# Performance work log

Measured on AMD Instinct MI355X. Metric: run time of the kernel, lower is better.

The kernel has to match this reference:

```python
import jax, jax.numpy as jnp
import numpy as np

N_HEAD = 16
SPARSITY_K = 64


def _apply_rope(x):
    # x: [B, H, T, D]
    D = x.shape[-1]
    T = x.shape[-2]
    freqs = 1.0 / (10000.0 ** (jnp.arange(0, D, 2, dtype=jnp.float32) / D))  # [D/2]
    angles = jnp.arange(T, dtype=jnp.float32)[:, None] * freqs[None, :]      # [T, D/2]
    cos, sin = jnp.cos(angles), jnp.sin(angles)
    xe, xo = x[..., ::2], x[..., 1::2]
    re = xe * cos - xo * sin
    ro = xe * sin + xo * cos
    return jnp.stack([re, ro], axis=-1).reshape(x.shape)


def _sparse_mask(route_weights, T, k):
    # Per head h, per query t: keep positions j<=t whose route score is among
    # the top-k of route_weights[h, 0:t+1] (tie-break by smaller index, like topk).
    s = route_weights[:, :T]                      # [H, T]
    idx = jnp.arange(T)
    # G[h, jp, j] = 1 if position jp beats position j in the top-k ordering
    G = (s[:, :, None] > s[:, None, :]) | ((s[:, :, None] == s[:, None, :]) & (idx[:, None] < idx[None, :]))
    rank = jnp.cumsum(G.astype(jnp.int32), axis=1)  # rank[h, t, j] = #{jp<=t beating j}
    causal = idx[None, :, None] >= idx[None, None, :]  # j <= t
    return causal & (rank < k)                    # [H, T, T] bool


def reference(x, W_attn, b_attn, W_proj, b_proj, route_weights):
    B, T, C = x.shape
    H = N_HEAD
    D = C // H
    qkv = x @ W_attn + b_attn                     # [B, T, 3C]
    q, k, v = jnp.split(qkv, 3, axis=-1)

    def heads(t):
        return t.reshape(B, T, H, D).transpose(0, 2, 1, 3)  # [B, H, T, D]

    q, k, v = heads(q), heads(k), heads(v)
    q = _apply_rope(q)
    k = _apply_rope(k)

    scores = jnp.einsum('bhtd,bhsd->bhts', q, k) / jnp.sqrt(jnp.float32(D))
    mask = _sparse_mask(route_weights, T, SPARSITY_K)       # [H, T, T]
    scores = jnp.where(mask[None], scores, -jnp.inf)
    attn = jax.nn.softmax(scores, axis=-1)                  # dropout off (eval mode)
    out = jnp.einsum('bhts,bhsd->bhtd', attn, v)
    out = out.transpose(0, 2, 1, 3).reshape(B, T, C)
    return out @ W_proj + b_proj


def setup_inputs() -> dict:
    key = jax.random.key(0)
    ks = jax.random.split(key, 6)
    B, T, C, H = 2, 2048, 2048, 16
    return {
        'x': jax.random.normal(ks[0], (B, T, C), dtype=jnp.float32),
        'W_attn': jax.random.normal(ks[1], (C, 3 * C), dtype=jnp.float32) * 0.02,
        'b_attn': jnp.zeros((3 * C,), dtype=jnp.float32),
        'W_proj': jax.random.normal(ks[2], (C, C), dtype=jnp.float32) * 0.02,
        'b_proj': jnp.zeros((C,), dtype=jnp.float32),
        'route_weights': jax.random.normal(ks[3], (H, T), dtype=jnp.float32) * 0.02,
    }
```

## Files before the change

### kernel.cpp

```cpp
#include <hip/hip_runtime.h>
#include <stdint.h>

#define B_ 2
#define T_ 2048
#define C_ 2048
#define H_ 16
#define D_ 128
#define KSP 64
#define C3 6144

typedef __attribute__((ext_vector_type(4))) float f32x4;
typedef __attribute__((ext_vector_type(8))) _Float16 f16x8;
typedef __attribute__((ext_vector_type(4))) _Float16 f16x4;
typedef __attribute__((ext_vector_type(2))) _Float16 f16x2;

__device__ __forceinline__ void gload16(const void* g, void* l) {
  __builtin_amdgcn_global_load_lds(
      (__attribute__((address_space(1))) void*)(uintptr_t)g,
      (__attribute__((address_space(3))) void*)(uint32_t)(uintptr_t)l,
      16, 0, 0);
}

__global__ void k_cvt(const float* __restrict__ in, _Float16* __restrict__ out, int n) {
  int i = (blockIdx.x * blockDim.x + threadIdx.x) * 4;
  if (i >= n) return;
  const float4 v = *(const float4*)(in + i);
  f16x4 o;
  o.x = (_Float16)v.x; o.y = (_Float16)v.y; o.z = (_Float16)v.z; o.w = (_Float16)v.w;
  *(f16x4*)(out + i) = o;
}

__global__ void k_tconv(const float* __restrict__ W, _Float16* __restrict__ WT, int K, int N) {
  __shared__ float tile[32][33];
  const int n0 = blockIdx.x * 32, k0 = blockIdx.y * 32;
  const int tx = threadIdx.x, ty = threadIdx.y;
#pragma unroll
  for (int r = 0; r < 4; ++r)
    tile[ty + r * 8][tx] = W[(size_t)(k0 + ty + r * 8) * N + n0 + tx];
  __syncthreads();
#pragma unroll
  for (int r = 0; r < 4; ++r)
    WT[(size_t)(n0 + ty + r * 8) * K + k0 + tx] = (_Float16)tile[tx][ty + r * 8];
}

template <int F16OUT, int NJ, int ROPE>
__global__ __launch_bounds__(512) void k_gemm256(const _Float16* __restrict__ A,
                                                 const _Float16* __restrict__ BT,
                                                 const float* __restrict__ bias,
                                                 void* __restrict__ Cout,
                                                 int M, int N, int K,
                                                 int RGC, int RH, int CW) {
  constexpr int BN = 64 * NJ;
  __shared__ __align__(16) _Float16 sA[2][256 * 64];
  __shared__ __align__(16) _Float16 sB[2][BN * 64];
  const int tid = threadIdx.x;
  const int lane = tid & 63;
  const int wid = tid >> 6;
  const int wr = wid >> 2;
  const int wc = wid & 3;
  const int lr = lane & 15;
  const int g = lane >> 4;
  const int rot = lr & 7;
  const int bid = blockIdx.x;
  const int x = bid & 7, q = bid >> 3;
  const int bm = (x / RGC) * RH + q / CW;
  const int bn = (x % RGC) * CW + q % CW;
  const size_t arow0 = (size_t)bm * 256;
  const size_t brow0 = (size_t)bn * BN;

  f32x4 acc[8][NJ];
#pragma unroll
  for (int mi = 0; mi < 8; ++mi)
#pragma unroll
    for (int nj = 0; nj < NJ; ++nj) acc[mi][nj] = (f32x4){0.f, 0.f, 0.f, 0.f};

  auto STAGE_A = [&](int slot, int k0) {
    const int rord[4] = {0, 2, 1, 3};
#pragma unroll
    for (int ri = 0; ri < 4; ++ri) {
      const int u = tid + rord[ri] * 512;
      const int row = u >> 3, grl = u & 7;
      const int grn = (grl - (row & 7)) & 7;
      gload16(A + (arow0 + row) * K + k0 + grn * 8, &sA[slot][u * 8]);
    }
  };
  auto STAGE_B = [&](int slot, int k0) {
#pragma unroll
    for (int r = 0; r < NJ; ++r) {
      const int u = tid + r * 512;
      const int row = u >> 3, grl = u & 7;
      const int grn = (grl - (row & 7)) & 7;
      gload16(BT + (brow0 + row) * K + k0 + grn * 8, &sB[slot][u * 8]);
    }
  };

  f16x8 af[4], bf[NJ];
  auto LDA = [&](int slot, int mh, int kk) {
#pragma unroll
    for (int mi = 0; mi < 4; ++mi) {
      const int row = wr * 128 + (mh * 4 + mi) * 16 + lr;
      af[mi] = *(const f16x8*)&sA[slot][row * 64 + (((kk * 4 + g + rot) & 7) << 3)];
    }
  };
  auto LDB = [&](int slot, int kk) {
#pragma unroll
    for (int nj = 0; nj < NJ; ++nj) {
      const int row = wc * (16 * NJ) + nj * 16 + lr;
      bf[nj] = *(const f16x8*)&sB[slot][row * 64 + (((kk * 4 + g + rot) & 7) << 3)];
    }
  };
  auto MFMAB = [&](int mh) {
    __builtin_amdgcn_s_setprio(1);
#pragma unroll
    for (int mi = 0; mi < 4; ++mi)
#pragma unroll
      for (int nj = 0; nj < NJ; ++nj)
        acc[mh * 4 + mi][nj] =
            __builtin_amdgcn_mfma_f32_16x16x32_f16(af[mi], bf[nj], acc[mh * 4 + mi][nj], 0, 0, 0);
    __builtin_amdgcn_s_setprio(0);
    __builtin_amdgcn_sched_barrier(0);
  };

  STAGE_B(0, 0);
  STAGE_A(0, 0);
  asm volatile("s_waitcnt vmcnt(2)" ::: "memory");
  __builtin_amdgcn_s_barrier();

  const int NT = K >> 6;
  for (int t = 0; t < NT; ++t) {
    const int s = t & 1, ns = s ^ 1;
    const bool pf = (t + 1 < NT);
    const int kn = (t + 1) << 6;
    LDB(s, 0);
    LDA(s, 0, 0);
    if (pf) STAGE_B(ns, kn);
    __builtin_amdgcn_s_barrier();
    asm volatile("s_waitcnt lgkmcnt(0)" ::: "memory");
    __builtin_amdgcn_sched_barrier(0);
    MFMAB(0);
    if (pf)
      asm volatile("s_waitcnt vmcnt(%0)" ::"i"(NJ) : "memory");
    else
      asm volatile("s_waitcnt vmcnt(0)" ::: "memory");
    __builtin_amdgcn_s_barrier();
    LDA(s, 1, 0);
    if (pf) STAGE_A(ns, kn);
    __builtin_amdgcn_s_barrier();
    asm volatile("s_waitcnt lgkmcnt(0)" ::: "memory");
    __builtin_amdgcn_sched_barrier(0);
    MFMAB(1);
    __builtin_amdgcn_s_barrier();
    LDB(s, 1);
    LDA(s, 0, 1);
    __builtin_amdgcn_s_barrier();
    asm volatile("s_waitcnt lgkmcnt(0)" ::: "memory");
    __builtin_amdgcn_sched_barrier(0);
    MFMAB(0);
    __builtin_amdgcn_s_barrier();
    LDA(s, 1, 1);
    __builtin_amdgcn_s_barrier();
    asm volatile("s_waitcnt lgkmcnt(0)" ::: "memory");
    __builtin_amdgcn_sched_barrier(0);
    MFMAB(1);
    if (pf)
      asm volatile("s_waitcnt vmcnt(2)" ::: "memory");
    __builtin_amdgcn_s_barrier();
  }
  const size_t row0 = arow0 + wr * 128;
  const size_t col0 = brow0 + wc * (16 * NJ);
  const float sgn = (lr & 1) ? 1.f : -1.f;
#pragma unroll
  for (int nj = 0; nj < NJ; ++nj) {
    const size_t colbase = col0 + nj * 16;
    const size_t col = colbase + lr;
    const float bv = bias[col];
    const bool dorope = ROPE && (colbase < 2 * C_);
    float freq = 0.f;
    if (dorope) {
      const int dp = ((int)(col & 127)) >> 1;
      freq = __expf(-0.14391156831212787f * (float)dp);
    }
#pragma unroll
    for (int mi = 0; mi < 8; ++mi) {
#pragma unroll
      for (int r = 0; r < 4; ++r) {
        const size_t row = row0 + mi * 16 + g * 4 + r;
        float v = acc[mi][nj][r] + bv;
        if (dorope) {
          const float pe = __shfl_xor(v, 1);
          float sn, cs;
          __sincosf((float)(int)(row & (T_ - 1)) * freq, &sn, &cs);
          v = v * cs + sgn * pe * sn;
        }
        if (F16OUT)
          ((_Float16*)Cout)[row * N + col] = (_Float16)v;
        else
          ((float*)Cout)[row * N + col] = v;
      }
    }
  }
}

__global__ __launch_bounds__(256) void k_death(const float* __restrict__ rw, int* __restrict__ dd) {
  const int widG = blockIdx.x * 4 + (threadIdx.x >> 6);
  const int lane = threadIdx.x & 63;
  const int h = widG >> 11, j = widG & (T_ - 1);
  const float* s = rw + h * T_;
  const float sj = s[j];
  int total = 0, d = T_;
  for (int base = 0; base < T_; base += 64) {
    const int t = base + lane;
    const float st = s[t];
    const bool beat = (st > sj) || (st == sj && t < j);
    const unsigned long long bal = __ballot(beat);
    const int c = __popcll(bal);
    if (total + c >= KSP) {
      const int need = KSP - total;
      const int p = __popcll(bal & ((1ull << lane) - 1ull));
      const unsigned long long win = __ballot(beat && (p == need - 1));
      d = base + __builtin_ctzll(win);
      break;
    }
    total += c;
  }
  if (lane == 0) dd[widG] = d;
}

__global__ __launch_bounds__(64) void k_slist(const int* __restrict__ dd,
                                              uint32_t* __restrict__ slist) {
  const int bid = blockIdx.x;
  const int qb = bid & 127, h = bid >> 7;
  const int i0 = qb * 16, i1 = i0 + 15;
  const int lane = threadIdx.x;
  const int* dh = dd + h * T_;
  uint32_t* lb = slist + (size_t)bid * 96;
  int total = 0;
  for (int base = 0; base <= i1; base += 64) {
    const int j = base + lane;
    const int dv = dh[j];
    const bool pred = (j <= i1) && (dv > i0);
    const unsigned long long bal = __ballot(pred);
    const int pos = total + __popcll(bal & ((1ull << lane) - 1ull));
    if (pred) lb[pos] = (uint32_t)j | ((uint32_t)dv << 12);
    total += __popcll(bal);
  }
  for (int s = total + lane; s < 96; s += 64) lb[s] = 0;
}

__global__ __launch_bounds__(64, 4) void k_mattn(const _Float16* __restrict__ qkv,
                                                 const uint32_t* __restrict__ slist,
                                                 _Float16* __restrict__ out) {
  __shared__ uint32_t jd[96];
  __shared__ int joff[96];
  __shared__ __align__(16) _Float16 Pl[16 * 104];
  __shared__ __align__(16) _Float16 VT[2048];
  const int bid = blockIdx.x;
  const int qb = bid & 127, h = (bid >> 7) & 15, b = bid >> 11;
  const int i0 = qb * 16;
  const int lane = threadIdx.x;
  const int g = lane >> 4, l = lane & 15;
  const uint32_t* lb = slist + (size_t)((h << 7) + qb) * 96;
  {
    const uint32_t pk = lb[lane];
    jd[lane] = pk;
    joff[lane] = (int)(pk & 0xFFFu) * C3;
    if (lane < 32) {
      const uint32_t pk1 = lb[64 + lane];
      jd[64 + lane] = pk1;
      joff[64 + lane] = (int)(pk1 & 0xFFFu) * C3;
    }
  }
  __syncthreads();
  const _Float16* qkvb = qkv + (size_t)b * T_ * C3;
  const _Float16* qrow = qkvb + (size_t)(i0 + l) * C3 + h * D_ + 8 * g;
  f16x8 bq[4];
#pragma unroll
  for (int c = 0; c < 4; ++c) bq[c] = *(const f16x8*)(qrow + 32 * c);
  f32x4 sacc[6];
  const _Float16* kbase = qkvb + C_ + h * D_ + 8 * g;
#pragma unroll
  for (int t = 0; t < 6; ++t) {
    const int jo = joff[16 * t + l];
    const _Float16* kr = kbase + jo;
    f16x8 ak[4];
#pragma unroll
    for (int c = 0; c < 4; ++c) ak[c] = *(const f16x8*)(kr + 32 * c);
    f32x4 a = {0.f, 0.f, 0.f, 0.f};
#pragma unroll
    for (int c = 0; c < 4; ++c)
      a = __builtin_amdgcn_mfma_f32_16x16x32_f16(ak[c], bq[c], a, 0, 0, 0);
    sacc[t] = a;
  }
  const int iq = i0 + l;
  float P[6][4];
  float m = -INFINITY;
#pragma unroll
  for (int t = 0; t < 6; ++t)
#pragma unroll
    for (int r = 0; r < 4; ++r) {
      const uint32_t pk = jd[16 * t + 4 * g + r];
      const int j = (int)(pk & 0xFFFu);
      const int d = (int)(pk >> 12);
      const bool ok = (j <= iq) && (d > iq);
      const float x = ok ? sacc[t][r] * 0.08838834764831845f : -INFINITY;
      P[t][r] = x;
      m = fmaxf(m, x);
    }
  m = fmaxf(m, __shfl_xor(m, 16));
  m = fmaxf(m, __shfl_xor(m, 32));
  float ssum = 0.f;
#pragma unroll
  for (int t = 0; t < 6; ++t)
#pragma unroll
    for (int r = 0; r < 4; ++r) {
      const float e = __expf(P[t][r] - m);
      P[t][r] = e;
      ssum += e;
    }
  ssum += __shfl_xor(ssum, 16);
  ssum += __shfl_xor(ssum, 32);
  const float inv = 1.0f / ssum;
#pragma unroll
  for (int t = 0; t < 6; ++t) {
    f16x4 w;
    w.x = (_Float16)(P[t][0] * inv);
    w.y = (_Float16)(P[t][1] * inv);
    w.z = (_Float16)(P[t][2] * inv);
    w.w = (_Float16)(P[t][3] * inv);
    *(f16x4*)&Pl[l * 104 + 16 * t + 4 * g] = w;
  }
  __syncthreads();
  f16x8 pf[3];
#pragma unroll
  for (int cc = 0; cc < 3; ++cc) pf[cc] = *(const f16x8*)&Pl[l * 104 + 32 * cc + 8 * g];
  f32x4 oacc[8];
#pragma unroll
  for (int mt = 0; mt < 8; ++mt) oacc[mt] = (f32x4){0.f, 0.f, 0.f, 0.f};
  const _Float16* vbase = qkvb + 2 * C_ + h * D_;
#pragma unroll
  for (int cc = 0; cc < 3; ++cc) {
    const int jo0 = joff[32 * cc + l];
    const int jo1 = joff[32 * cc + 16 + l];
#pragma unroll
    for (int dh = 0; dh < 2; ++dh) {
      f16x8 vl0[2], vl1[2];
#pragma unroll
      for (int cp = 0; cp < 2; ++cp) {
        vl0[cp] = *(const f16x8*)(vbase + jo0 + 64 * dh + 32 * cp + 8 * g);
        vl1[cp] = *(const f16x8*)(vbase + jo1 + 64 * dh + 32 * cp + 8 * g);
      }
      __syncthreads();
#pragma unroll
      for (int tau = 0; tau < 2; ++tau)
#pragma unroll
        for (int cp = 0; cp < 2; ++cp) {
          const int mtl = 2 * cp + (g >> 1);
          const int lt0 = 8 * (g & 1);
          const int gt = (2 * tau + (l >> 3)) ^ g;
          const int et = l & 7;
#pragma unroll
          for (int e = 0; e < 8; ++e) {
            const int idx = ((mtl * 16 + lt0 + e) * 4 + gt) * 8 + et;
            VT[idx] = tau ? vl1[cp][e] : vl0[cp][e];
          }
        }
      __syncthreads();
#pragma unroll
      for (int mtl = 0; mtl < 4; ++mtl) {
        const int sgr = (l >> 3) | ((mtl & 1) << 1);
        const f16x8 vf = *(const f16x8*)&VT[((mtl * 16 + l) * 4 + (g ^ sgr)) * 8];
        oacc[4 * dh + mtl] =
            __builtin_amdgcn_mfma_f32_16x16x32_f16(pf[cc], vf, oacc[4 * dh + mtl], 0, 0, 0);
      }
    }
  }
  _Float16* ob = out + (size_t)(b * T_ + i0 + 4 * g) * C_ + h * D_ + l;
#pragma unroll
  for (int mt = 0; mt < 8; ++mt)
#pragma unroll
    for (int r = 0; r < 4; ++r)
      ob[(size_t)r * C_ + 16 * mt] = (_Float16)oacc[mt][r];
}

extern "C" void kernel_launch(void* const* d_in, const int* in_sizes, int n_in,
                              void* d_out, int out_size, void* d_ws, size_t ws_size,
                              hipStream_t stream) {
  const float* x  = (const float*)d_in[0];
  const float* Wa = (const float*)d_in[1];
  const float* ba = (const float*)d_in[2];
  const float* Wp = (const float*)d_in[3];
  const float* bp = (const float*)d_in[4];
  const float* rw = (const float*)d_in[5];

  char* ws = (char*)d_ws;
  _Float16* qkv16 = (_Float16*)(ws);
  _Float16* WaT   = (_Float16*)(ws + (size_t)48 * 1024 * 1024);
  _Float16* WpT   = (_Float16*)(ws + (size_t)72 * 1024 * 1024);
  _Float16* x16   = (_Float16*)(ws + (size_t)80 * 1024 * 1024);
  int* dd  = (int*)(ws + (size_t)96 * 1024 * 1024);
  uint32_t* slist = (uint32_t*)(ws + (size_t)96 * 1024 * 1024 + (2 << 17));
  _Float16* att16 = x16;

  k_cvt<<<dim3((B_ * T_ * C_) / 1024), dim3(256), 0, stream>>>(x, x16, B_ * T_ * C_);
  k_tconv<<<dim3(C3 / 32, C_ / 32), dim3(32, 8), 0, stream>>>(Wa, WaT, C_, C3);
  k_tconv<<<dim3(C_ / 32, C_ / 32), dim3(32, 8), 0, stream>>>(Wp, WpT, C_, C_);
  k_gemm256<1, 3, 1><<<dim3(512), dim3(512), 0, stream>>>(
      x16, WaT, ba, (void*)qkv16, B_ * T_, C3, C_, 4, 8, 8);
  k_death<<<dim3(H_ * T_ / 4), dim3(256), 0, stream>>>(rw, dd);
  k_slist<<<dim3(H_ * (T_ / 16)), dim3(64), 0, stream>>>(dd, slist);
  k_mattn<<<dim3(B_ * H_ * (T_ / 16)), dim3(64), 0, stream>>>(qkv16, slist, att16);
  k_gemm256<0, 2, 0><<<dim3(256), dim3(512), 0, stream>>>(
      att16, WpT, bp, d_out, B_ * T_, C_, C_, 4, 8, 4);
}
```

Measured before the change: 243.0 us.

## Stage fp16 GEMM epilogue through LDS and compute RoPE via angle recurrence

The fp16-output GEMM epilogue now writes results into shared memory, which reuses the A/B staging buffers, and then stores them to global memory as coalesced 16-byte vectors. Previously each lane wrote scattered 2-byte elements. RoPE sin/cos values are now produced by rotation recurrences from a few __sincosf calls instead of one per element, which reduces transcendental work. The costs are an extra barrier and LDS round trip, plus small float drift from the recurrence across 128 rows.

```diff
diff --git a/kernel.cpp b/kernel.cpp
--- a/kernel.cpp
+++ b/kernel.cpp
@@ -51,8 +51,11 @@
                                                  int M, int N, int K,
                                                  int RGC, int RH, int CW) {
   constexpr int BN = 64 * NJ;
-  __shared__ __align__(16) _Float16 sA[2][256 * 64];
-  __shared__ __align__(16) _Float16 sB[2][BN * 64];
+  constexpr int ABYTES = 2 * 256 * 64 * 2;
+  constexpr int BBYTES = 2 * BN * 64 * 2;
+  __shared__ __align__(16) char smem[ABYTES + BBYTES];
+  _Float16* sA = (_Float16*)smem;
+  _Float16* sB = (_Float16*)(smem + ABYTES);
   const int tid = threadIdx.x;
   const int lane = tid & 63;
   const int wid = tid >> 6;
@@ -81,7 +84,7 @@
       const int u = tid + rord[ri] * 512;
       const int row = u >> 3, grl = u & 7;
       const int grn = (grl - (row & 7)) & 7;
-      gload16(A + (arow0 + row) * K + k0 + grn * 8, &sA[slot][u * 8]);
+      gload16(A + (arow0 + row) * K + k0 + grn * 8, &sA[slot * 16384 + u * 8]);
     }
   };
   auto STAGE_B = [&](int slot, int k0) {
@@ -90,7 +93,7 @@
       const int u = tid + r * 512;
       const int row = u >> 3, grl = u & 7;
       const int grn = (grl - (row & 7)) & 7;
-      gload16(BT + (brow0 + row) * K + k0 + grn * 8, &sB[slot][u * 8]);
+      gload16(BT + (brow0 + row) * K + k0 + grn * 8, &sB[slot * (BN * 64) + u * 8]);
     }
   };
 
@@ -99,14 +102,14 @@
 #pragma unroll
     for (int mi = 0; mi < 4; ++mi) {
       const int row = wr * 128 + (mh * 4 + mi) * 16 + lr;
-      af[mi] = *(const f16x8*)&sA[slot][row * 64 + (((kk * 4 + g + rot) & 7) << 3)];
+      af[mi] = *(const f16x8*)&sA[slot * 16384 + row * 64 + (((kk * 4 + g + rot) & 7) << 3)];
     }
   };
   auto LDB = [&](int slot, int kk) {
 #pragma unroll
     for (int nj = 0; nj < NJ; ++nj) {
       const int row = wc * (16 * NJ) + nj * 16 + lr;
-      bf[nj] = *(const f16x8*)&sB[slot][row * 64 + (((kk * 4 + g + rot) & 7) << 3)];
+      bf[nj] = *(const f16x8*)&sB[slot * (BN * 64) + row * 64 + (((kk * 4 + g + rot) & 7) << 3)];
     }
   };
   auto MFMAB = [&](int mh) {
@@ -166,36 +169,71 @@
       asm volatile("s_waitcnt vmcnt(2)" ::: "memory");
     __builtin_amdgcn_s_barrier();
   }
+  __builtin_amdgcn_sched_barrier(0);
   const size_t row0 = arow0 + wr * 128;
   const size_t col0 = brow0 + wc * (16 * NJ);
   const float sgn = (lr & 1) ? 1.f : -1.f;
-#pragma unroll
-  for (int nj = 0; nj < NJ; ++nj) {
-    const size_t colbase = col0 + nj * 16;
-    const size_t col = colbase + lr;
-    const float bv = bias[col];
-    const bool dorope = ROPE && (colbase < 2 * C_);
-    float freq = 0.f;
-    if (dorope) {
-      const int dp = ((int)(col & 127)) >> 1;
-      freq = __expf(-0.14391156831212787f * (float)dp);
-    }
+  if (F16OUT) {
+    constexpr int CLP = BN + 8;
+    _Float16* Cl = (_Float16*)smem;
+    const int t_base = ((int)(row0 & (T_ - 1))) + g * 4;
+#pragma unroll
+    for (int nj = 0; nj < NJ; ++nj) {
+      const size_t colbase = col0 + nj * 16;
+      const int col = (int)colbase + lr;
+      const float bv = bias[col];
+      const bool dorope = ROPE && (colbase < 2 * C_);
+      float c1 = 1.f, s1 = 0.f, c16 = 1.f, s16 = 0.f, cm = 1.f, sm = 0.f;
+      if (dorope) {
+        const float freq = __expf(-0.14391156831212787f * (float)((col & 127) >> 1));
+        __sincosf((float)t_base * freq, &sm, &cm);
+        __sincosf(freq, &s1, &c1);
+        __sincosf(16.f * freq, &s16, &c16);
+      }
+#pragma unroll
+      for (int mi = 0; mi < 8; ++mi) {
+        float cr = cm, sr = sm;
+#pragma unroll
+        for (int r = 0; r < 4; ++r) {
+          const int rowL = wr * 128 + mi * 16 + g * 4 + r;
+          float v = acc[mi][nj][r] + bv;
+          if (dorope) {
+            const float pe = __shfl_xor(v, 1);
+            v = v * cr + sgn * pe * sr;
+            const float nc = cr * c1 - sr * s1;
+            sr = sr * c1 + cr * s1;
+            cr = nc;
+          }
+          Cl[rowL * CLP + wc * (16 * NJ) + nj * 16 + lr] = (_Float16)v;
+        }
+        if (dorope) {
+          const float nc = cm * c16 - sm * s16;
+          sm = sm * c16 + cm * s16;
+          cm = nc;
+        }
+      }
+    }
+    __syncthreads();
+    constexpr int CPR = BN / 8;
+#pragma unroll
+    for (int rr = 0; rr < (256 * CPR) / 512; ++rr) {
+      const int u = tid + rr * 512;
+      const int row = u / CPR, ch = u % CPR;
+      *(f16x8*)((_Float16*)Cout + (arow0 + row) * N + brow0 + ch * 8) =
+          *(const f16x8*)&Cl[row * CLP + ch * 8];
+    }
+  } else {
 #pragma unroll
     for (int mi = 0; mi < 8; ++mi) {
 #pragma unroll
-      for (int r = 0; r < 4; ++r) {
-        const size_t row = row0 + mi * 16 + g * 4 + r;
-        float v = acc[mi][nj][r] + bv;
-        if (dorope) {
-          const float pe = __shfl_xor(v, 1);
-          float sn, cs;
-          __sincosf((float)(int)(row & (T_ - 1)) * freq, &sn, &cs);
-          v = v * cs + sgn * pe * sn;
+      for (int nj = 0; nj < NJ; ++nj) {
+        const size_t col = col0 + nj * 16 + lr;
+        const float bv = bias[col];
+#pragma unroll
+        for (int r = 0; r < 4; ++r) {
+          const size_t row = row0 + mi * 16 + g * 4 + r;
+          ((float*)Cout)[row * N + col] = acc[mi][nj][r] + bv;
         }
-        if (F16OUT)
-          ((_Float16*)Cout)[row * N + col] = (_Float16)v;
-        else
-          ((float*)Cout)[row * N + col] = v;
       }
     }
   }
```

After: 245.5 us. Within noise of the previous version (+1.1%).

## Split QKV GEMM into RoPE and non-RoPE launches; compute RoPE by angle recurrence

Applied to the files above, without the earlier changes.

The QKV projection GEMM is split into two launches: one covering the Q and K columns with RoPE enabled, and one covering the V columns with RoPE compiled out. The wide NJ template value is raised from 3 to 4, and the grid sizes change to match. In the epilogue, the per-element sincos is replaced by three sincos calls per column plus rotation recurrences across rows. This cuts transcendental work and removes the runtime RoPE branch, at the cost of an extra kernel launch, a different tile shape, and some accumulated rounding error in the recurrence.

```diff
diff --git a/kernel.cpp b/kernel.cpp
--- a/kernel.cpp
+++ b/kernel.cpp
@@ -169,33 +169,41 @@
   const size_t row0 = arow0 + wr * 128;
   const size_t col0 = brow0 + wc * (16 * NJ);
   const float sgn = (lr & 1) ? 1.f : -1.f;
+  const int t0 = ((int)(row0 & (T_ - 1))) + g * 4;
 #pragma unroll
   for (int nj = 0; nj < NJ; ++nj) {
-    const size_t colbase = col0 + nj * 16;
-    const size_t col = colbase + lr;
+    const size_t col = col0 + nj * 16 + lr;
     const float bv = bias[col];
-    const bool dorope = ROPE && (colbase < 2 * C_);
-    float freq = 0.f;
-    if (dorope) {
-      const int dp = ((int)(col & 127)) >> 1;
-      freq = __expf(-0.14391156831212787f * (float)dp);
+    float c1 = 1.f, s1 = 0.f, c16 = 1.f, s16 = 0.f, cm = 1.f, sm = 0.f;
+    if (ROPE) {
+      const float freq = __expf(-0.14391156831212787f * (float)(((int)col & 127) >> 1));
+      __sincosf((float)t0 * freq, &sm, &cm);
+      __sincosf(freq, &s1, &c1);
+      __sincosf(16.f * freq, &s16, &c16);
     }
 #pragma unroll
     for (int mi = 0; mi < 8; ++mi) {
+      float cr = cm, sr = sm;
 #pragma unroll
       for (int r = 0; r < 4; ++r) {
         const size_t row = row0 + mi * 16 + g * 4 + r;
         float v = acc[mi][nj][r] + bv;
-        if (dorope) {
+        if (ROPE) {
           const float pe = __shfl_xor(v, 1);
-          float sn, cs;
-          __sincosf((float)(int)(row & (T_ - 1)) * freq, &sn, &cs);
-          v = v * cs + sgn * pe * sn;
+          v = v * cr + sgn * pe * sr;
+          const float nc = cr * c1 - sr * s1;
+          sr = sr * c1 + cr * s1;
+          cr = nc;
         }
         if (F16OUT)
           ((_Float16*)Cout)[row * N + col] = (_Float16)v;
         else
           ((float*)Cout)[row * N + col] = v;
+      }
+      if (ROPE) {
+        const float nc = cm * c16 - sm * s16;
+        sm = sm * c16 + cm * s16;
+        cm = nc;
       }
     }
   }
@@ -404,8 +412,11 @@
   k_cvt<<<dim3((B_ * T_ * C_) / 1024), dim3(256), 0, stream>>>(x, x16, B_ * T_ * C_);
   k_tconv<<<dim3(C3 / 32, C_ / 32), dim3(32, 8), 0, stream>>>(Wa, WaT, C_, C3);
   k_tconv<<<dim3(C_ / 32, C_ / 32), dim3(32, 8), 0, stream>>>(Wp, WpT, C_, C_);
-  k_gemm256<1, 3, 1><<<dim3(512), dim3(512), 0, stream>>>(
-      x16, WaT, ba, (void*)qkv16, B_ * T_, C3, C_, 4, 8, 8);
+  k_gemm256<1, 4, 1><<<dim3(256), dim3(512), 0, stream>>>(
+      x16, WaT, ba, (void*)qkv16, B_ * T_, C3, C_, 4, 8, 4);
+  k_gemm256<1, 4, 0><<<dim3(128), dim3(512), 0, stream>>>(
+      x16, WaT + (size_t)4096 * C_, ba + 4096, (void*)(qkv16 + 4096),
+      B_ * T_, C3, C_, 4, 8, 2);
   k_death<<<dim3(H_ * T_ / 4), dim3(256), 0, stream>>>(rw, dd);
   k_slist<<<dim3(H_ * (T_ / 16)), dim3(64), 0, stream>>>(dd, slist);
   k_mattn<<<dim3(B_ * H_ * (T_ / 16)), dim3(64), 0, stream>>>(qkv16, slist, att16);
```

New measurement: 258.2 us. +6.3%, slower.
